# Performance work log

Hardware: AMD Instinct MI355X
Metric: run time of the kernel (lower is better)

Reference implementation:

```python
import jax, jax.numpy as jnp
import numpy as np

VOCAB = 50000
D = 256       # text_latent_size
E = 20000     # num_of_evidences
L = 20        # words_in_question / words per evidence sentence


def position_encoding(L, D):
    # encoding[i, j] = 1 - i/L - (j/D) * (1 - 2*i/L)
    i = jnp.arange(L, dtype=jnp.float32)[:, None] / L
    j = jnp.arange(D, dtype=jnp.float32)[None, :] / D
    return 1.0 - i - j * (1.0 - 2.0 * i)  # [L, D]


def setup_inputs() -> dict:
    key = jax.random.key(0)
    ks = jax.random.split(key, 8)
    evidence = jax.random.randint(ks[0], (E, L), 0, VOCAB)
    question = jax.random.randint(ks[1], (1, L), 0, VOCAB)
    scale = 0.05
    q_table = jax.random.normal(ks[2], (VOCAB, D), dtype=jnp.float32) * scale
    e_table = jax.random.normal(ks[3], (VOCAB, D), dtype=jnp.float32) * scale
    te1 = jax.random.normal(ks[4], (E, D), dtype=jnp.float32) * scale
    te2 = jax.random.normal(ks[5], (E, D), dtype=jnp.float32) * scale
    W = jax.random.normal(ks[6], (VOCAB, D), dtype=jnp.float32) * scale
    b = jax.random.normal(ks[7], (VOCAB,), dtype=jnp.float32) * scale
    return {"evidence": evidence, "question": question, "q_table": q_table,
            "e_table": e_table, "te1": te1, "te2": te2, "W": W, "b": b}


def reference(evidence, question, q_table, e_table, te1, te2, W, b):
    pe = position_encoding(L, D)                            # [L, D]
    # question: embed, position-encode, sum over words -> [D]
    q_emb = (q_table[question[0]] * pe).sum(axis=0)         # [D]
    # evidence: two embeddings, position-encode, sum over words -> [E, D]
    ev_comp = (q_table[evidence] * pe[None]).sum(axis=1) + te2  # [E, D]
    ev_feat = (e_table[evidence] * pe[None]).sum(axis=1) + te1  # [E, D]
    # attention over memories
    scores = ev_comp @ q_emb                                 # [E]
    weights = jax.nn.softmax(scores)                         # [E]
    weighted = weights @ ev_feat                             # [D]
    features = weighted + q_emb                              # [D]
    logits = features @ W.T + b                              # [VOCAB]
    return jax.nn.softmax(logits)
```

## Files before the change

kernel.cpp:

```cpp
#include <hip/hip_runtime.h>

#define D      256
#define L_W    20
#define E_CNT  20000
#define VOCAB  50000
#define TOTROW (VOCAB + E_CNT)

#define CHUNK   1024
#define NCHUNK  49
#define NSLICE  4
#define RPS     (E_CNT / NSLICE)
#define PSTRIDE (NCHUNK * CHUNK)

#define K6_BLOCKS 512
#define K6_STRIDE 768

#define OFF_QEMB  0
#define OFF_X     256
#define OFF_Y     512
#define OFF_WTE1  768
#define OFF_SWP   1024
#define OFF_LP    1536
#define OFF_A     2560
#define OFF_B     (OFF_A + VOCAB)
#define OFF_P     (OFF_B + VOCAB)
#define OFF_Q     (OFF_P + VOCAB)
#define OFF_EXPW  (OFF_Q + VOCAB)
#define OFF_EXPL  (OFF_EXPW + E_CNT)
#define OFF_PPART (OFF_EXPL + VOCAB)
#define OFF_QPART (OFF_PPART + NSLICE * PSTRIDE)
#define OFF_XYP   (OFF_QPART + NSLICE * PSTRIDE)
#define WS_FLOATS (OFF_XYP + K6_BLOCKS * K6_STRIDE)

__device__ __forceinline__ float wave_reduce(float v) {
#pragma unroll
    for (int o = 32; o > 0; o >>= 1) v += __shfl_xor(v, o, 64);
    return v;
}

__device__ __forceinline__ float u_of(int j) { return 1.f - (float)j * (1.f / 128.f); }
__device__ __forceinline__ float s_of(int j) { return (float)j * (1.f / 256.f); }

__global__ void k1_qemb(const int* __restrict__ question,
                        const float* __restrict__ q_table,
                        float* __restrict__ ws) {
    __shared__ int sQ[L_W];
    int tid = threadIdx.x;
    if (tid < L_W) sQ[tid] = question[tid];
    __syncthreads();
    int j = tid;
    float u = u_of(j), s = s_of(j);
    float acc = 0.f;
#pragma unroll
    for (int i = 0; i < L_W; ++i) {
        float a = 1.f - (float)i * (1.f / (float)L_W);
        acc += q_table[(size_t)sQ[i] * D + j] * (a * u + s);
    }
    ws[OFF_QEMB + j] = acc;
}

__global__ void k2_ab(const float* __restrict__ q_table, float* __restrict__ ws) {
    __shared__ float sQE[D];
    int tid = threadIdx.x;
    sQE[tid] = ws[OFF_QEMB + tid];
    __syncthreads();
    int wv = tid >> 6, lane = tid & 63;
    int v = blockIdx.x * 4 + wv;
    int j0 = lane * 4;
    const float4 q = *reinterpret_cast<const float4*>(&q_table[(size_t)v * D + j0]);
    float qe0 = sQE[j0], qe1 = sQE[j0 + 1], qe2 = sQE[j0 + 2], qe3 = sQE[j0 + 3];
    float accA = q.x * (u_of(j0) * qe0) + q.y * (u_of(j0 + 1) * qe1) +
                 q.z * (u_of(j0 + 2) * qe2) + q.w * (u_of(j0 + 3) * qe3);
    float accB = q.x * (s_of(j0) * qe0) + q.y * (s_of(j0 + 1) * qe1) +
                 q.z * (s_of(j0 + 2) * qe2) + q.w * (s_of(j0 + 3) * qe3);
    accA = wave_reduce(accA);
    accB = wave_reduce(accB);
    if (lane == 0) {
        ws[OFF_A + v] = accA;
        ws[OFF_B + v] = accB;
        ws[OFF_P + v] = 0.f;
        ws[OFF_Q + v] = 0.f;
    }
}

__global__ void k3_scores(const int* __restrict__ evidence,
                          const float* __restrict__ te2,
                          float* __restrict__ ws) {
    __shared__ float sQE[D];
    __shared__ float sPart[4];
    int tid = threadIdx.x;
    sQE[tid] = ws[OFF_QEMB + tid];
    __syncthreads();
    int wv = tid >> 6, lane = tid & 63;
    int gw = blockIdx.x * 4 + wv;
    int stride = gridDim.x * 4;
    int j0 = lane * 4;
    const float4 qe = *reinterpret_cast<const float4*>(&sQE[j0]);
    float wsum = 0.f;
    for (int e = gw; e < E_CNT; e += stride) {
        const float4 t = *reinterpret_cast<const float4*>(&te2[(size_t)e * D + j0]);
        float p = t.x * qe.x + t.y * qe.y + t.z * qe.z + t.w * qe.w;
        if (lane < 2 * L_W) {
            int l = (lane < L_W) ? lane : (lane - L_W);
            int idx = evidence[e * L_W + l];
            if (lane < L_W) {
                float a = 1.f - (float)l * (1.f / (float)L_W);
                p += a * ws[OFF_A + idx];
            } else {
                p += ws[OFF_B + idx];
            }
        }
        float s_e = wave_reduce(p);
        float ex = expf(s_e);
        if (lane == 0) ws[OFF_EXPW + e] = ex;
        wsum += ex;
    }
    if (lane == 0) sPart[wv] = wsum;
    __syncthreads();
    if (tid == 0) ws[OFF_SWP + blockIdx.x] = sPart[0] + sPart[1] + sPart[2] + sPart[3];
}

__global__ void k5_scatter2(const int* __restrict__ evidence, float* __restrict__ ws) {
    __shared__ float sP[CHUNK], sQ[CHUNK];
    int tid = threadIdx.x;
    int chunk = blockIdx.x % NCHUNK;
    int slice = blockIdx.x / NCHUNK;
    for (int i = tid; i < CHUNK; i += 256) { sP[i] = 0.f; sQ[i] = 0.f; }
    __syncthreads();
    int lo = chunk * CHUNK;
    int r0 = slice * RPS;
    for (int r = tid; r < RPS; r += 256) {
        int e = r0 + r;
        float w = ws[OFF_EXPW + e];
        const int4* rp = reinterpret_cast<const int4*>(evidence + (size_t)e * L_W);
        int4 v0 = rp[0], v1 = rp[1], v2 = rp[2], v3 = rp[3], v4 = rp[4];
        int idxs[L_W] = {v0.x, v0.y, v0.z, v0.w, v1.x, v1.y, v1.z, v1.w,
                         v2.x, v2.y, v2.z, v2.w, v3.x, v3.y, v3.z, v3.w,
                         v4.x, v4.y, v4.z, v4.w};
#pragma unroll
        for (int l = 0; l < L_W; ++l) {
            int d = idxs[l] - lo;
            if ((unsigned)d < (unsigned)CHUNK) {
                float a = 1.f - (float)l * (1.f / (float)L_W);
                atomicAdd(&sP[d], w * a);
                atomicAdd(&sQ[d], w);
            }
        }
    }
    __syncthreads();
    float* pp = &ws[OFF_PPART + (size_t)slice * PSTRIDE + (size_t)chunk * CHUNK];
    float* qp = &ws[OFF_QPART + (size_t)slice * PSTRIDE + (size_t)chunk * CHUNK];
    for (int i = tid; i < CHUNK; i += 256) { pp[i] = sP[i]; qp[i] = sQ[i]; }
}

__global__ void k5b_reduce(float* __restrict__ ws) {
    int v = blockIdx.x * 256 + threadIdx.x;
    if (v < VOCAB) {
        float p = 0.f, q = 0.f;
#pragma unroll
        for (int s = 0; s < NSLICE; ++s) {
            p += ws[OFF_PPART + s * PSTRIDE + v];
            q += ws[OFF_QPART + s * PSTRIDE + v];
        }
        ws[OFF_P + v] = p;
        ws[OFF_Q + v] = q;
    }
}

__global__ void k5_scatter(const int* __restrict__ evidence, float* __restrict__ ws) {
    int tid = threadIdx.x;
    int wv = tid >> 6, lane = tid & 63;
    int gw = blockIdx.x * 4 + wv;
    int stride = gridDim.x * 4;
    for (int e = gw; e < E_CNT; e += stride) {
        float w = ws[OFF_EXPW + e];
        if (lane < L_W) {
            int idx = evidence[e * L_W + lane];
            float a = 1.f - (float)lane * (1.f / (float)L_W);
            atomicAdd(&ws[OFF_P + idx], w * a);
            atomicAdd(&ws[OFF_Q + idx], w);
        }
    }
}

__global__ void k6_xyt(const float* __restrict__ e_table,
                       const float* __restrict__ te1,
                       float* __restrict__ ws) {
    __shared__ float sAcc[K6_STRIDE];
    int tid = threadIdx.x;
    for (int i = tid; i < K6_STRIDE; i += 256) sAcc[i] = 0.f;
    __syncthreads();
    int wv = tid >> 6, lane = tid & 63;
    int gw = blockIdx.x * 4 + wv;
    int nw = gridDim.x * 4;
    int j0 = lane * 4;
    float x0 = 0.f, x1 = 0.f, x2 = 0.f, x3 = 0.f;
    float y0 = 0.f, y1 = 0.f, y2 = 0.f, y3 = 0.f;
    float t0 = 0.f, t1 = 0.f, t2 = 0.f, t3 = 0.f;
    for (int v0 = gw * 4; v0 < TOTROW; v0 += nw * 4) {
        if (v0 < VOCAB) {
            const float4 P4 = *reinterpret_cast<const float4*>(&ws[OFF_P + v0]);
            const float4 Q4 = *reinterpret_cast<const float4*>(&ws[OFF_Q + v0]);
            const float4 r0 = *reinterpret_cast<const float4*>(&e_table[(size_t)(v0 + 0) * D + j0]);
            const float4 r1 = *reinterpret_cast<const float4*>(&e_table[(size_t)(v0 + 1) * D + j0]);
            const float4 r2 = *reinterpret_cast<const float4*>(&e_table[(size_t)(v0 + 2) * D + j0]);
            const float4 r3 = *reinterpret_cast<const float4*>(&e_table[(size_t)(v0 + 3) * D + j0]);
            x0 += P4.x * r0.x + P4.y * r1.x + P4.z * r2.x + P4.w * r3.x;
            x1 += P4.x * r0.y + P4.y * r1.y + P4.z * r2.y + P4.w * r3.y;
            x2 += P4.x * r0.z + P4.y * r1.z + P4.z * r2.z + P4.w * r3.z;
            x3 += P4.x * r0.w + P4.y * r1.w + P4.z * r2.w + P4.w * r3.w;
            y0 += Q4.x * r0.x + Q4.y * r1.x + Q4.z * r2.x + Q4.w * r3.x;
            y1 += Q4.x * r0.y + Q4.y * r1.y + Q4.z * r2.y + Q4.w * r3.y;
            y2 += Q4.x * r0.z + Q4.y * r1.z + Q4.z * r2.z + Q4.w * r3.z;
            y3 += Q4.x * r0.w + Q4.y * r1.w + Q4.z * r2.w + Q4.w * r3.w;
        } else {
            int e0 = v0 - VOCAB;
            const float4 W4 = *reinterpret_cast<const float4*>(&ws[OFF_EXPW + e0]);
            const float4 r0 = *reinterpret_cast<const float4*>(&te1[(size_t)(e0 + 0) * D + j0]);
            const float4 r1 = *reinterpret_cast<const float4*>(&te1[(size_t)(e0 + 1) * D + j0]);
            const float4 r2 = *reinterpret_cast<const float4*>(&te1[(size_t)(e0 + 2) * D + j0]);
            const float4 r3 = *reinterpret_cast<const float4*>(&te1[(size_t)(e0 + 3) * D + j0]);
            t0 += W4.x * r0.x + W4.y * r1.x + W4.z * r2.x + W4.w * r3.x;
            t1 += W4.x * r0.y + W4.y * r1.y + W4.z * r2.y + W4.w * r3.y;
            t2 += W4.x * r0.z + W4.y * r1.z + W4.z * r2.z + W4.w * r3.z;
            t3 += W4.x * r0.w + W4.y * r1.w + W4.z * r2.w + W4.w * r3.w;
        }
    }
    atomicAdd(&sAcc[j0 + 0], x0); atomicAdd(&sAcc[j0 + 1], x1);
    atomicAdd(&sAcc[j0 + 2], x2); atomicAdd(&sAcc[j0 + 3], x3);
    atomicAdd(&sAcc[256 + j0 + 0], y0); atomicAdd(&sAcc[256 + j0 + 1], y1);
    atomicAdd(&sAcc[256 + j0 + 2], y2); atomicAdd(&sAcc[256 + j0 + 3], y3);
    atomicAdd(&sAcc[512 + j0 + 0], t0); atomicAdd(&sAcc[512 + j0 + 1], t1);
    atomicAdd(&sAcc[512 + j0 + 2], t2); atomicAdd(&sAcc[512 + j0 + 3], t3);
    __syncthreads();
    float* base = &ws[OFF_XYP + (size_t)blockIdx.x * K6_STRIDE];
    for (int i = tid; i < K6_STRIDE; i += 256) base[i] = sAcc[i];
}

__global__ void k6b_reduce(float* __restrict__ ws) {
    __shared__ float sR[256 * 4];
    int tid = threadIdx.x;
    int s0 = blockIdx.x * 4;
    float a0 = 0.f, a1 = 0.f, a2 = 0.f, a3 = 0.f;
#pragma unroll
    for (int r = 0; r < K6_BLOCKS / 256; ++r) {
        int b = tid + r * 256;
        const float4 v = *reinterpret_cast<const float4*>(&ws[OFF_XYP + (size_t)b * K6_STRIDE + s0]);
        a0 += v.x; a1 += v.y; a2 += v.z; a3 += v.w;
    }
    sR[tid * 4 + 0] = a0; sR[tid * 4 + 1] = a1;
    sR[tid * 4 + 2] = a2; sR[tid * 4 + 3] = a3;
    __syncthreads();
#pragma unroll
    for (int off = 128; off > 0; off >>= 1) {
        if (tid < off) {
#pragma unroll
            for (int c = 0; c < 4; ++c) sR[tid * 4 + c] += sR[(tid + off) * 4 + c];
        }
        __syncthreads();
    }
    if (tid < 4) {
        int s = s0 + tid;
        float v = sR[tid];
        if (s < 256)      ws[OFF_X + s] = v;
        else if (s < 512) ws[OFF_Y + s - 256] = v;
        else              ws[OFF_WTE1 + s - 512] = v;
    }
}

__global__ void k8_logits(const float* __restrict__ Wm, const float* __restrict__ bv,
                          float* __restrict__ ws) {
    __shared__ float sF[D];
    __shared__ float sRed[256];
    __shared__ float sPart[4];
    int tid = threadIdx.x;
    sRed[tid] = ws[OFF_SWP + tid] + ws[OFF_SWP + 256 + tid];
    __syncthreads();
#pragma unroll
    for (int off = 128; off > 0; off >>= 1) {
        if (tid < off) sRed[tid] += sRed[tid + off];
        __syncthreads();
    }
    float invw = 1.f / sRed[0];
    sF[tid] = (u_of(tid) * ws[OFF_X + tid] + s_of(tid) * ws[OFF_Y + tid] +
               ws[OFF_WTE1 + tid]) * invw + ws[OFF_QEMB + tid];
    __syncthreads();
    int wv = tid >> 6, lane = tid & 63;
    int gw = blockIdx.x * 4 + wv;
    int stride = gridDim.x * 4;
    int j0 = lane * 4;
    const float4 f = *reinterpret_cast<const float4*>(&sF[j0]);
    float lsum = 0.f;
    for (int v = gw; v < VOCAB; v += stride) {
        const float4 w4 = *reinterpret_cast<const float4*>(&Wm[(size_t)v * D + j0]);
        float p = w4.x * f.x + w4.y * f.y + w4.z * f.z + w4.w * f.w;
        float logit = wave_reduce(p) + bv[v];
        float ex = expf(logit);
        if (lane == 0) ws[OFF_EXPL + v] = ex;
        lsum += ex;
    }
    if (lane == 0) sPart[wv] = lsum;
    __syncthreads();
    if (tid == 0) ws[OFF_LP + blockIdx.x] = sPart[0] + sPart[1] + sPart[2] + sPart[3];
}

__global__ void k10_norm(float* __restrict__ out, const float* __restrict__ ws) {
    __shared__ float sRed[256];
    int tid = threadIdx.x;
    float l = 0.f;
#pragma unroll
    for (int r = 0; r < 4; ++r) l += ws[OFF_LP + tid + r * 256];
    sRed[tid] = l;
    __syncthreads();
#pragma unroll
    for (int off = 128; off > 0; off >>= 1) {
        if (tid < off) sRed[tid] += sRed[tid + off];
        __syncthreads();
    }
    float invL = 1.f / sRed[0];
    int i = blockIdx.x * 256 + tid;
    if (i < VOCAB) out[i] = ws[OFF_EXPL + i] * invL;
}

extern "C" void kernel_launch(void* const* d_in, const int* in_sizes, int n_in,
                              void* d_out, int out_size, void* d_ws, size_t ws_size,
                              hipStream_t stream) {
    const int*   evidence = (const int*)d_in[0];
    const int*   question = (const int*)d_in[1];
    const float* q_table  = (const float*)d_in[2];
    const float* e_table  = (const float*)d_in[3];
    const float* te1      = (const float*)d_in[4];
    const float* te2      = (const float*)d_in[5];
    const float* Wm       = (const float*)d_in[6];
    const float* bv       = (const float*)d_in[7];
    float* out = (float*)d_out;
    float* ws  = (float*)d_ws;

    const bool big = ws_size >= (size_t)WS_FLOATS * sizeof(float);

    k1_qemb<<<1, 256, 0, stream>>>(question, q_table, ws);
    k2_ab<<<VOCAB / 4, 256, 0, stream>>>(q_table, ws);
    k3_scores<<<512, 256, 0, stream>>>(evidence, te2, ws);
    if (big) {
        k5_scatter2<<<NCHUNK * NSLICE, 256, 0, stream>>>(evidence, ws);
        k5b_reduce<<<(VOCAB + 255) / 256, 256, 0, stream>>>(ws);
    } else {
        k5_scatter<<<512, 256, 0, stream>>>(evidence, ws);
    }
    k6_xyt<<<K6_BLOCKS, 256, 0, stream>>>(e_table, te1, ws);
    k6b_reduce<<<K6_STRIDE / 4, 256, 0, stream>>>(ws);
    k8_logits<<<1024, 256, 0, stream>>>(Wm, bv, ws);
    k10_norm<<<(VOCAB + 255) / 256, 256, 0, stream>>>(out, ws);
}
```

Before: 256.6 us.

## Fuse qemb into A/B kernel, fold slice reduction into k6, use 16-lane row groups

```diff
diff --git a/kernel.cpp b/kernel.cpp
--- a/kernel.cpp
+++ b/kernel.cpp
@@ -37,49 +37,59 @@
     for (int o = 32; o > 0; o >>= 1) v += __shfl_xor(v, o, 64);
     return v;
 }
+__device__ __forceinline__ float group16_reduce(float v) {
+#pragma unroll
+    for (int o = 1; o < 16; o <<= 1) v += __shfl_xor(v, o, 64);
+    return v;
+}
 
 __device__ __forceinline__ float u_of(int j) { return 1.f - (float)j * (1.f / 128.f); }
 __device__ __forceinline__ float s_of(int j) { return (float)j * (1.f / 256.f); }
 
-__global__ void k1_qemb(const int* __restrict__ question,
-                        const float* __restrict__ q_table,
-                        float* __restrict__ ws) {
+__global__ void k2_ab(const int* __restrict__ question,
+                      const float* __restrict__ q_table,
+                      float* __restrict__ ws) {
     __shared__ int sQ[L_W];
+    __shared__ float sQE[D];
     int tid = threadIdx.x;
     if (tid < L_W) sQ[tid] = question[tid];
     __syncthreads();
-    int j = tid;
-    float u = u_of(j), s = s_of(j);
-    float acc = 0.f;
-#pragma unroll
-    for (int i = 0; i < L_W; ++i) {
-        float a = 1.f - (float)i * (1.f / (float)L_W);
-        acc += q_table[(size_t)sQ[i] * D + j] * (a * u + s);
-    }
-    ws[OFF_QEMB + j] = acc;
-}
-
-__global__ void k2_ab(const float* __restrict__ q_table, float* __restrict__ ws) {
-    __shared__ float sQE[D];
-    int tid = threadIdx.x;
-    sQE[tid] = ws[OFF_QEMB + tid];
-    __syncthreads();
-    int wv = tid >> 6, lane = tid & 63;
-    int v = blockIdx.x * 4 + wv;
-    int j0 = lane * 4;
-    const float4 q = *reinterpret_cast<const float4*>(&q_table[(size_t)v * D + j0]);
-    float qe0 = sQE[j0], qe1 = sQE[j0 + 1], qe2 = sQE[j0 + 2], qe3 = sQE[j0 + 3];
-    float accA = q.x * (u_of(j0) * qe0) + q.y * (u_of(j0 + 1) * qe1) +
-                 q.z * (u_of(j0 + 2) * qe2) + q.w * (u_of(j0 + 3) * qe3);
-    float accB = q.x * (s_of(j0) * qe0) + q.y * (s_of(j0 + 1) * qe1) +
-                 q.z * (s_of(j0 + 2) * qe2) + q.w * (s_of(j0 + 3) * qe3);
-    accA = wave_reduce(accA);
-    accB = wave_reduce(accB);
-    if (lane == 0) {
-        ws[OFF_A + v] = accA;
-        ws[OFF_B + v] = accB;
-        ws[OFF_P + v] = 0.f;
-        ws[OFF_Q + v] = 0.f;
+    {
+        float u = u_of(tid), s = s_of(tid);
+        float acc = 0.f;
+#pragma unroll
+        for (int i = 0; i < L_W; ++i) {
+            float a = 1.f - (float)i * (1.f / (float)L_W);
+            acc += q_table[(size_t)sQ[i] * D + tid] * (a * u + s);
+        }
+        sQE[tid] = acc;
+        if (blockIdx.x == 0) ws[OFF_QEMB + tid] = acc;
+    }
+    __syncthreads();
+    int wv = tid >> 6, lane = tid & 63, g = lane >> 4, li = lane & 15;
+    int gw = blockIdx.x * 4 + wv, nw = gridDim.x * 4;
+    for (int v0 = gw * 4; v0 < VOCAB; v0 += nw * 4) {
+        int row = v0 + g;
+        const float* rp = q_table + (size_t)row * D;
+        float accA = 0.f, accB = 0.f;
+#pragma unroll
+        for (int c = 0; c < 4; ++c) {
+            int j = c * 64 + li * 4;
+            const float4 q  = *reinterpret_cast<const float4*>(rp + j);
+            const float4 qe = *reinterpret_cast<const float4*>(&sQE[j]);
+            accA += q.x * (u_of(j + 0) * qe.x) + q.y * (u_of(j + 1) * qe.y) +
+                    q.z * (u_of(j + 2) * qe.z) + q.w * (u_of(j + 3) * qe.w);
+            accB += q.x * (s_of(j + 0) * qe.x) + q.y * (s_of(j + 1) * qe.y) +
+                    q.z * (s_of(j + 2) * qe.z) + q.w * (s_of(j + 3) * qe.w);
+        }
+        accA = group16_reduce(accA);
+        accB = group16_reduce(accB);
+        if (li == 0) {
+            ws[OFF_A + row] = accA;
+            ws[OFF_B + row] = accB;
+            ws[OFF_P + row] = 0.f;
+            ws[OFF_Q + row] = 0.f;
+        }
     }
 }
 
@@ -91,30 +101,36 @@
     int tid = threadIdx.x;
     sQE[tid] = ws[OFF_QEMB + tid];
     __syncthreads();
-    int wv = tid >> 6, lane = tid & 63;
-    int gw = blockIdx.x * 4 + wv;
-    int stride = gridDim.x * 4;
-    int j0 = lane * 4;
-    const float4 qe = *reinterpret_cast<const float4*>(&sQE[j0]);
+    int wv = tid >> 6, lane = tid & 63, g = lane >> 4, li = lane & 15;
+    int gw = blockIdx.x * 4 + wv, nw = gridDim.x * 4;
     float wsum = 0.f;
-    for (int e = gw; e < E_CNT; e += stride) {
-        const float4 t = *reinterpret_cast<const float4*>(&te2[(size_t)e * D + j0]);
-        float p = t.x * qe.x + t.y * qe.y + t.z * qe.z + t.w * qe.w;
-        if (lane < 2 * L_W) {
-            int l = (lane < L_W) ? lane : (lane - L_W);
-            int idx = evidence[e * L_W + l];
-            if (lane < L_W) {
-                float a = 1.f - (float)l * (1.f / (float)L_W);
-                p += a * ws[OFF_A + idx];
-            } else {
-                p += ws[OFF_B + idx];
+    for (int e0 = gw * 4; e0 < E_CNT; e0 += nw * 4) {
+        int e = e0 + g;
+        const float* tp = te2 + (size_t)e * D;
+        float p = 0.f;
+#pragma unroll
+        for (int c = 0; c < 4; ++c) {
+            int j = c * 64 + li * 4;
+            const float4 t  = *reinterpret_cast<const float4*>(tp + j);
+            const float4 qe = *reinterpret_cast<const float4*>(&sQE[j]);
+            p += t.x * qe.x + t.y * qe.y + t.z * qe.z + t.w * qe.w;
+        }
+        {
+            int idx = evidence[e * L_W + li];
+            float a = 1.f - (float)li * (1.f / (float)L_W);
+            p += a * ws[OFF_A + idx] + ws[OFF_B + idx];
+            if (li < L_W - 16) {
+                int w2 = li + 16;
+                int idx2 = evidence[e * L_W + w2];
+                float a2 = 1.f - (float)w2 * (1.f / (float)L_W);
+                p += a2 * ws[OFF_A + idx2] + ws[OFF_B + idx2];
             }
         }
-        float s_e = wave_reduce(p);
-        float ex = expf(s_e);
-        if (lane == 0) ws[OFF_EXPW + e] = ex;
-        wsum += ex;
-    }
+        p = group16_reduce(p);
+        float ex = expf(p);
+        if (li == 0) { ws[OFF_EXPW + e] = ex; wsum += ex; }
+    }
+    wsum = wave_reduce(wsum);
     if (lane == 0) sPart[wv] = wsum;
     __syncthreads();
     if (tid == 0) ws[OFF_SWP + blockIdx.x] = sPart[0] + sPart[1] + sPart[2] + sPart[3];
@@ -153,20 +169,6 @@
     for (int i = tid; i < CHUNK; i += 256) { pp[i] = sP[i]; qp[i] = sQ[i]; }
 }
 
-__global__ void k5b_reduce(float* __restrict__ ws) {
-    int v = blockIdx.x * 256 + threadIdx.x;
-    if (v < VOCAB) {
-        float p = 0.f, q = 0.f;
-#pragma unroll
-        for (int s = 0; s < NSLICE; ++s) {
-            p += ws[OFF_PPART + s * PSTRIDE + v];
-            q += ws[OFF_QPART + s * PSTRIDE + v];
-        }
-        ws[OFF_P + v] = p;
-        ws[OFF_Q + v] = q;
-    }
-}
-
 __global__ void k5_scatter(const int* __restrict__ evidence, float* __restrict__ ws) {
     int tid = threadIdx.x;
     int wv = tid >> 6, lane = tid & 63;
@@ -185,6 +187,9 @@
 
 __global__ void k6_xyt(const float* __restrict__ e_table,
                        const float* __restrict__ te1,
+                       const float* __restrict__ Pp,
+                       const float* __restrict__ Qp,
+                       int nslice,
                        float* __restrict__ ws) {
     __shared__ float sAcc[K6_STRIDE];
     int tid = threadIdx.x;
@@ -199,8 +204,14 @@
     float t0 = 0.f, t1 = 0.f, t2 = 0.f, t3 = 0.f;
     for (int v0 = gw * 4; v0 < TOTROW; v0 += nw * 4) {
         if (v0 < VOCAB) {
-            const float4 P4 = *reinterpret_cast<const float4*>(&ws[OFF_P + v0]);
-            const float4 Q4 = *reinterpret_cast<const float4*>(&ws[OFF_Q + v0]);
+            float4 P4 = make_float4(0.f, 0.f, 0.f, 0.f);
+            float4 Q4 = make_float4(0.f, 0.f, 0.f, 0.f);
+            for (int s = 0; s < nslice; ++s) {
+                const float4 ps = *reinterpret_cast<const float4*>(Pp + (size_t)s * PSTRIDE + v0);
+                const float4 qs = *reinterpret_cast<const float4*>(Qp + (size_t)s * PSTRIDE + v0);
+                P4.x += ps.x; P4.y += ps.y; P4.z += ps.z; P4.w += ps.w;
+                Q4.x += qs.x; Q4.y += qs.y; Q4.z += qs.z; Q4.w += qs.w;
+            }
             const float4 r0 = *reinterpret_cast<const float4*>(&e_table[(size_t)(v0 + 0) * D + j0]);
             const float4 r1 = *reinterpret_cast<const float4*>(&e_table[(size_t)(v0 + 1) * D + j0]);
             const float4 r2 = *reinterpret_cast<const float4*>(&e_table[(size_t)(v0 + 2) * D + j0]);
@@ -285,20 +296,25 @@
     sF[tid] = (u_of(tid) * ws[OFF_X + tid] + s_of(tid) * ws[OFF_Y + tid] +
                ws[OFF_WTE1 + tid]) * invw + ws[OFF_QEMB + tid];
     __syncthreads();
-    int wv = tid >> 6, lane = tid & 63;
-    int gw = blockIdx.x * 4 + wv;
-    int stride = gridDim.x * 4;
-    int j0 = lane * 4;
-    const float4 f = *reinterpret_cast<const float4*>(&sF[j0]);
+    int wv = tid >> 6, lane = tid & 63, g = lane >> 4, li = lane & 15;
+    int gw = blockIdx.x * 4 + wv, nw = gridDim.x * 4;
     float lsum = 0.f;
-    for (int v = gw; v < VOCAB; v += stride) {
-        const float4 w4 = *reinterpret_cast<const float4*>(&Wm[(size_t)v * D + j0]);
-        float p = w4.x * f.x + w4.y * f.y + w4.z * f.z + w4.w * f.w;
-        float logit = wave_reduce(p) + bv[v];
-        float ex = expf(logit);
-        if (lane == 0) ws[OFF_EXPL + v] = ex;
-        lsum += ex;
-    }
+    for (int v0 = gw * 4; v0 < VOCAB; v0 += nw * 4) {
+        int row = v0 + g;
+        const float* wp = Wm + (size_t)row * D;
+        float p = 0.f;
+#pragma unroll
+        for (int c = 0; c < 4; ++c) {
+            int j = c * 64 + li * 4;
+            const float4 w4 = *reinterpret_cast<const float4*>(wp + j);
+            const float4 f4 = *reinterpret_cast<const float4*>(&sF[j]);
+            p += w4.x * f4.x + w4.y * f4.y + w4.z * f4.z + w4.w * f4.w;
+        }
+        p = group16_reduce(p);
+        float ex = expf(p + bv[row]);
+        if (li == 0) { ws[OFF_EXPL + row] = ex; lsum += ex; }
+    }
+    lsum = wave_reduce(lsum);
     if (lane == 0) sPart[wv] = lsum;
     __syncthreads();
     if (tid == 0) ws[OFF_LP + blockIdx.x] = sPart[0] + sPart[1] + sPart[2] + sPart[3];
@@ -338,16 +354,17 @@
 
     const bool big = ws_size >= (size_t)WS_FLOATS * sizeof(float);
 
-    k1_qemb<<<1, 256, 0, stream>>>(question, q_table, ws);
-    k2_ab<<<VOCAB / 4, 256, 0, stream>>>(q_table, ws);
+    k2_ab<<<1024, 256, 0, stream>>>(question, q_table, ws);
     k3_scores<<<512, 256, 0, stream>>>(evidence, te2, ws);
     if (big) {
         k5_scatter2<<<NCHUNK * NSLICE, 256, 0, stream>>>(evidence, ws);
-        k5b_reduce<<<(VOCAB + 255) / 256, 256, 0, stream>>>(ws);
+        k6_xyt<<<K6_BLOCKS, 256, 0, stream>>>(e_table, te1,
+                                              &ws[OFF_PPART], &ws[OFF_QPART], NSLICE, ws);
     } else {
         k5_scatter<<<512, 256, 0, stream>>>(evidence, ws);
-    }
-    k6_xyt<<<K6_BLOCKS, 256, 0, stream>>>(e_table, te1, ws);
+        k6_xyt<<<K6_BLOCKS, 256, 0, stream>>>(e_table, te1,
+                                              &ws[OFF_P], &ws[OFF_Q], 1, ws);
+    }
     k6b_reduce<<<K6_STRIDE / 4, 256, 0, stream>>>(ws);
     k8_logits<<<1024, 256, 0, stream>>>(Wm, bv, ws);
     k10_norm<<<(VOCAB + 255) / 256, 256, 0, stream>>>(out, ws);
```

New measurement: 249.9 us. 2.6% less time.
